# Optimization experiments

Measured on AMD Instinct MI355X. Metric: run time of the kernel, lower is better.

The kernel has to match this reference:

```python
import jax, jax.numpy as jnp
import numpy as np

B, S, R, C_Q, C_KV, H, C_A = 1, 128, 256, 256, 256, 8, 32


def setup_inputs() -> dict:
    key = jax.random.key(0)
    ks = jax.random.split(key, 11)
    scale = 0.02
    q = jax.random.normal(ks[0], (B, S, R, C_Q), jnp.float32)
    kv = jax.random.normal(ks[1], (B, S, R, C_KV), jnp.float32)
    bias = jax.random.normal(ks[2], (B, 1, R, R, H), jnp.float32)
    bias_mask = jax.random.randint(ks[3], (B, S, R), 0, 2).astype(jnp.float32)
    w_q = jax.random.normal(ks[4], (C_Q, H, C_A), jnp.float32) * scale
    w_k = jax.random.normal(ks[5], (C_KV, H, C_A), jnp.float32) * scale
    w_v = jax.random.normal(ks[6], (C_KV, H, C_A), jnp.float32) * scale
    w_g = jax.random.normal(ks[7], (C_Q, H, C_A), jnp.float32) * scale
    b_g = jax.random.normal(ks[8], (H, C_A), jnp.float32) * scale
    w_o = jax.random.normal(ks[9], (H, C_A, C_Q), jnp.float32) * scale
    b_o = jax.random.normal(ks[10], (C_Q,), jnp.float32) * scale
    return {"q": q, "kv": kv, "bias": bias, "bias_mask": bias_mask,
            "w_q": w_q, "w_k": w_k, "w_v": w_v, "w_g": w_g, "b_g": b_g,
            "w_o": w_o, "b_o": b_o}


def reference(q, kv, bias, bias_mask, w_q, w_k, w_v, w_g, b_g, w_o, b_o):
    # q, kv: [B, S, R, C]; attention over residue dim R within each row s.
    c_a = w_q.shape[-1]
    normsize = 1.0 / jnp.sqrt(jnp.asarray(c_a, q.dtype))
    Q = jnp.einsum('bsqc,chd->bsqhd', q, w_q) * normsize  # [B,S,R,H,Ca]
    K = jnp.einsum('bskc,chd->bskhd', kv, w_k)
    V = jnp.einsum('bskc,chd->bskhd', kv, w_v)
    # affinity: [B,S,Q,K,H]
    AT = jnp.einsum('bsqhd,bskhd->bsqkh', Q, K)
    mask_bias = (bias_mask[:, :, None, :, None] - 1.0) * 1e9  # [B,S,1,K,1]
    AT = AT + bias + mask_bias
    AT = jax.nn.softmax(AT, axis=-2)  # softmax over K
    O = jnp.einsum('bsqkh,bskhd->bsqhd', AT, V)
    G = jax.nn.sigmoid(jnp.einsum('bsqc,chd->bsqhd', q, w_g) + b_g)
    O = O * G
    out = jnp.einsum('bsqhd,hdc->bsqc', O, w_o) + b_o  # [B,S,R,C_Q]
    return out
```

## Files before the change

### kernel.cpp

```cpp
#include <hip/hip_runtime.h>

typedef __bf16 bf16;
typedef __bf16 bf16x8 __attribute__((ext_vector_type(8)));
typedef __bf16 bf16x4 __attribute__((ext_vector_type(4)));
typedef float  f32x4  __attribute__((ext_vector_type(4)));
typedef unsigned int u32;
typedef unsigned int u32x2 __attribute__((ext_vector_type(2)));
typedef unsigned int u32x4 __attribute__((ext_vector_type(4)));
typedef unsigned short u16;

#define MFMA16(a, b, c) __builtin_amdgcn_mfma_f32_16x16x32_bf16((a), (b), (c), 0, 0, 0)
#define L2E 1.4426950408889634f


typedef __attribute__((address_space(3))) u32 lds_u32;
typedef const __attribute__((address_space(1))) u32 glob_u32;
__device__ __forceinline__ void gll16(const void* g, void* l) {
    __builtin_amdgcn_global_load_lds((glob_u32*)g, (lds_u32*)l, 16, 0, 0);
}

__device__ __forceinline__ u32 pk2(float lo, float hi) {
    u16 a = __builtin_bit_cast(u16, (bf16)lo);
    u16 b = __builtin_bit_cast(u16, (bf16)hi);
    return ((u32)b << 16) | (u32)a;
}

__device__ __forceinline__ float fexp2(float x) {
#if __has_builtin(__builtin_amdgcn_exp2f)
    return __builtin_amdgcn_exp2f(x);
#else
    return exp2f(x);
#endif
}

__global__ __launch_bounds__(256) void prep_kernel(
    const float* __restrict__ q, const float* __restrict__ kv,
    const float* __restrict__ bias,
    const float* __restrict__ w_q, const float* __restrict__ w_k,
    const float* __restrict__ w_v, const float* __restrict__ w_g,
    const float* __restrict__ w_o,
    bf16* __restrict__ qbf, bf16* __restrict__ kvbf, float* __restrict__ biasT,
    bf16* __restrict__ Wqg, bf16* __restrict__ Wkv, bf16* __restrict__ Wo)
{
    const float norm = 0.17677669529663687f * L2E;
    const int gid = blockIdx.x * 256 + threadIdx.x;
    const int gsz = gridDim.x * 256;

    for (int u = gid; u < 2097152; u += gsz) {
        const float* src; bf16* dst;
        if (u < 1048576) { src = q + (size_t)u * 8;            dst = qbf  + (size_t)u * 8; }
        else             { src = kv + (size_t)(u - 1048576)*8; dst = kvbf + (size_t)(u - 1048576)*8; }
        float4 x0 = *(const float4*)(src);
        float4 x1 = *(const float4*)(src + 4);
        bf16x8 t;
        t[0]=(bf16)x0.x; t[1]=(bf16)x0.y; t[2]=(bf16)x0.z; t[3]=(bf16)x0.w;
        t[4]=(bf16)x1.x; t[5]=(bf16)x1.y; t[6]=(bf16)x1.z; t[7]=(bf16)x1.w;
        *(bf16x8*)dst = t;
    }
    for (int u = gid; u < 524288; u += gsz) {
        int h = u >> 16, qq = (u >> 8) & 255, kk = u & 255;
        biasT[u] = bias[(((qq << 8) + kk) << 3) + h] * L2E;
    }
    for (int u = gid; u < 131072; u += gsz) {
        int n = u >> 8, k = u & 255;
        float v = (n < 256) ? w_q[k * 256 + n] * norm : w_g[k * 256 + (n - 256)];
        Wqg[u] = (bf16)v;
    }
    for (int u = gid; u < 131072; u += gsz) {
        int n = u >> 8, k = u & 255;
        float v = (n < 256) ? w_k[k * 256 + n] : w_v[k * 256 + (n - 256)];
        Wkv[u] = (bf16)v;
    }
    for (int u = gid; u < 65536; u += gsz) {
        int n = u >> 8, k = u & 255;
        Wo[u] = (bf16)w_o[k * 256 + n];
    }
}

template<bool F32OUT>
__device__ __forceinline__ void gemm_core(
    const bf16* __restrict__ A, const bf16* __restrict__ Bw,
    bf16* __restrict__ Cb, float* __restrict__ Cf, const float* __restrict__ bo,
    int m0, int n0, int ntot)
{
    __shared__ __align__(16) bf16 As[128 * 32];
    __shared__ __align__(16) bf16 Bs[128 * 32];

    const int tid  = threadIdx.x;
    const int lane = tid & 63, wave = tid >> 6;
    const int quad = lane >> 4, lc = lane & 15;
    const int wr = wave >> 1, wc = wave & 1;

    const int r0 = tid >> 2, p0 = tid & 3;
    const bf16* gA0 = A  + (size_t)(m0 + r0) * 256 + p0 * 8;
    const bf16* gA1 = A  + (size_t)(m0 + 64 + r0) * 256 + p0 * 8;
    const bf16* gB0 = Bw + (size_t)(n0 + r0) * 256 + p0 * 8;
    const bf16* gB1 = Bw + (size_t)(n0 + 64 + r0) * 256 + p0 * 8;
    bf16* lA0 = As + tid * 8;
    bf16* lA1 = As + (tid + 256) * 8;
    bf16* lB0 = Bs + tid * 8;
    bf16* lB1 = Bs + (tid + 256) * 8;

    f32x4 acc[4][4];
    #pragma unroll
    for (int i = 0; i < 4; ++i)
        #pragma unroll
        for (int j = 0; j < 4; ++j) acc[i][j] = f32x4{0.f, 0.f, 0.f, 0.f};

    #pragma unroll 1
    for (int kb = 0; kb < 8; ++kb) {
        const int ko = kb * 32;
        gll16(gA0 + ko, lA0);
        gll16(gA1 + ko, lA1);
        gll16(gB0 + ko, lB0);
        gll16(gB1 + ko, lB1);
        __syncthreads();

        bf16x8 aF[4], bF[4];
        #pragma unroll
        for (int mt = 0; mt < 4; ++mt)
            aF[mt] = *(const bf16x8*)(As + (wr * 64 + mt * 16 + lc) * 32 + quad * 8);
        #pragma unroll
        for (int nt = 0; nt < 4; ++nt)
            bF[nt] = *(const bf16x8*)(Bs + (wc * 64 + nt * 16 + lc) * 32 + quad * 8);
        #pragma unroll
        for (int mt = 0; mt < 4; ++mt)
            #pragma unroll
            for (int nt = 0; nt < 4; ++nt)
                acc[mt][nt] = MFMA16(aF[mt], bF[nt], acc[mt][nt]);
        __syncthreads();
    }

    #pragma unroll
    for (int mt = 0; mt < 4; ++mt) {
        #pragma unroll
        for (int nt = 0; nt < 4; ++nt) {
            const int row = m0 + wr * 64 + mt * 16 + quad * 4;
            const int col = n0 + wc * 64 + nt * 16 + lc;
            if (F32OUT) {
                float b = bo[col];
                #pragma unroll
                for (int rr = 0; rr < 4; ++rr)
                    Cf[(size_t)(row + rr) * ntot + col] = acc[mt][nt][rr] + b;
            } else {
                #pragma unroll
                for (int rr = 0; rr < 4; ++rr)
                    Cb[(size_t)(row + rr) * ntot + col] = (bf16)acc[mt][nt][rr];
            }
        }
    }
}

__global__ __launch_bounds__(256) void proj_kernel(
    const bf16* __restrict__ qbf, const bf16* __restrict__ kvbf,
    const bf16* __restrict__ Wqg, const bf16* __restrict__ Wkv,
    bf16* __restrict__ QG, bf16* __restrict__ KV)
{
    int bid = blockIdx.x;
    bool sel = bid >= 1024;
    int b = sel ? bid - 1024 : bid;
    int m0 = (b & 255) * 128, n0 = (b >> 8) * 128;
    gemm_core<false>(sel ? kvbf : qbf, sel ? Wkv : Wqg,
                     sel ? KV : QG, nullptr, nullptr, m0, n0, 512);
}

__global__ __launch_bounds__(256) void outproj_kernel(
    const bf16* __restrict__ OG, const bf16* __restrict__ Wo,
    const float* __restrict__ bo, float* __restrict__ out)
{
    int b = blockIdx.x;
    int m0 = (b & 255) * 128, n0 = (b >> 8) * 128;
    gemm_core<true>(OG, Wo, nullptr, out, bo, m0, n0, 256);
}

#define A_OFF_MASK 0
#define A_OFF_K    1024
#define A_OFF_VT   21504
#define A_LDS_TOT  (21504 + 32 * 264 * 2)

__global__ __launch_bounds__(256) void attn_kernel(
    const bf16* __restrict__ QG, const bf16* __restrict__ KV,
    const float* __restrict__ biasT, const float* __restrict__ bias_mask,
    const float* __restrict__ b_g, bf16* __restrict__ OG)
{
    __shared__ __align__(16) char smem[A_LDS_TOT];
    float* maskadd = (float*)(smem + A_OFF_MASK);
    bf16*  Ks      = (bf16*)(smem + A_OFF_K);
    bf16*  Vt      = (bf16*)(smem + A_OFF_VT);

    const int tid  = threadIdx.x;
    const int wave = tid >> 6, lane = tid & 63;
    const int quad = lane >> 4, lc = lane & 15;
    const int h = blockIdx.x >> 7;
    const int s = blockIdx.x & 127;

    maskadd[tid] = (bias_mask[s * 256 + tid] - 1.0f) * (1e9f * L2E);
    {
        const bf16* kvrow = KV + (size_t)(s * 256 + tid) * 512 + h * 32;
        #pragma unroll
        for (int j = 0; j < 4; ++j)
            *(bf16x8*)(Ks + tid * 40 + j * 8) = *(const bf16x8*)(kvrow + j * 8);
        bf16x8 vx[4];
        #pragma unroll
        for (int j = 0; j < 4; ++j) vx[j] = *(const bf16x8*)(kvrow + 256 + j * 8);
        #pragma unroll
        for (int d = 0; d < 32; ++d)
            Vt[d * 264 + tid] = vx[d >> 3][d & 7];
    }
    __syncthreads();

    #pragma unroll 1
    for (int p = 0; p < 4; ++p) {
        const int q0 = (wave * 4 + p) * 16;

        bf16x8 qf = *(const bf16x8*)(QG + (size_t)(s * 256 + q0 + lc) * 512 + h * 32 + quad * 8);

        const float* bT = biasT + (((size_t)h * 256 + q0 + lc) << 8) + quad * 4;
        u32x2 cw[16];
        float sum = 0.f;
        #pragma unroll
        for (int half = 0; half < 2; ++half) {
            f32x4 sc[8];
            #pragma unroll
            for (int k8 = 0; k8 < 8; ++k8) {
                const int kt = half * 8 + k8;
                bf16x8 kf = *(const bf16x8*)(Ks + (kt * 16 + lc) * 40 + quad * 8);
                f32x4 z = {0.f, 0.f, 0.f, 0.f};
                sc[k8] = MFMA16(kf, qf, z);
            }
            #pragma unroll
            for (int k8 = 0; k8 < 8; ++k8) {
                const int kt = half * 8 + k8;
                f32x4 bv = *(const f32x4*)(bT + kt * 16);
                f32x4 mv = *(const f32x4*)(maskadd + kt * 16 + quad * 4);
                float e0 = fexp2(sc[k8][0] + bv[0] + mv[0]);
                float e1 = fexp2(sc[k8][1] + bv[1] + mv[1]);
                float e2 = fexp2(sc[k8][2] + bv[2] + mv[2]);
                float e3 = fexp2(sc[k8][3] + bv[3] + mv[3]);
                sum += (e0 + e1) + (e2 + e3);
                cw[kt] = u32x2{pk2(e0, e1), pk2(e2, e3)};
            }
            __builtin_amdgcn_sched_barrier(0);
        }

        const bf16* gp = QG + (size_t)(s * 256 + q0 + lc) * 512 + 256 + h * 32 + quad * 4;
        bf16x4 gv0 = *(const bf16x4*)(gp);
        bf16x4 gv1 = *(const bf16x4*)(gp + 16);

        f32x4 o0 = {0.f, 0.f, 0.f, 0.f}, o1 = {0.f, 0.f, 0.f, 0.f};
        #pragma unroll
        for (int ks = 0; ks < 8; ++ks) {
            u32 c0 = cw[2 * ks].x,     c1 = cw[2 * ks].y;
            u32 c2 = cw[2 * ks + 1].x, c3 = cw[2 * ks + 1].y;
            u32x2 s02 = __builtin_amdgcn_permlane32_swap(c0, c2, false, false);
            u32x2 s13 = __builtin_amdgcn_permlane32_swap(c1, c3, false, false);
            u32x2 e02 = __builtin_amdgcn_permlane16_swap(s02.x, s02.y, false, false);
            u32x2 e13 = __builtin_amdgcn_permlane16_swap(s13.x, s13.y, false, false);
            u32x4 pw = {e02.x, e13.x, e02.y, e13.y};
            bf16x8 pf = __builtin_bit_cast(bf16x8, pw);
            bf16x8 v0 = *(const bf16x8*)(Vt + lc * 264 + ks * 32 + quad * 8);
            bf16x8 v1 = *(const bf16x8*)(Vt + (16 + lc) * 264 + ks * 32 + quad * 8);
            o0 = MFMA16(v0, pf, o0);
            o1 = MFMA16(v1, pf, o1);
        }

        sum += __shfl_xor(sum, 16, 64);
        sum += __shfl_xor(sum, 32, 64);
        const float inv = 1.0f / sum;

        const f32x4 bg0 = *(const f32x4*)(b_g + h * 32 + quad * 4);
        const f32x4 bg1 = *(const f32x4*)(b_g + h * 32 + 16 + quad * 4);
        bf16* op = OG + (size_t)(s * 256 + q0 + lc) * 256 + h * 32 + quad * 4;
        #pragma unroll
        for (int nt = 0; nt < 2; ++nt) {
            f32x4 ov = nt ? o1 : o0;
            f32x4 bg = nt ? bg1 : bg0;
            bf16x4 gv = nt ? gv1 : gv0;
            bf16x4 ob;
            #pragma unroll
            for (int rr = 0; rr < 4; ++rr) {
                float g = 1.0f / (1.0f + __expf(-((float)gv[rr] + bg[rr])));
                ob[rr] = (bf16)(ov[rr] * inv * g);
            }
            *(bf16x4*)(op + nt * 16) = ob;
        }
    }
}

extern "C" void kernel_launch(void* const* d_in, const int* in_sizes, int n_in,
                              void* d_out, int out_size, void* d_ws, size_t ws_size,
                              hipStream_t stream)
{
    (void)in_sizes; (void)n_in; (void)out_size; (void)ws_size;
    const float* q    = (const float*)d_in[0];
    const float* kv   = (const float*)d_in[1];
    const float* bias = (const float*)d_in[2];
    const float* mask = (const float*)d_in[3];
    const float* w_q  = (const float*)d_in[4];
    const float* w_k  = (const float*)d_in[5];
    const float* w_v  = (const float*)d_in[6];
    const float* w_g  = (const float*)d_in[7];
    const float* b_g  = (const float*)d_in[8];
    const float* w_o  = (const float*)d_in[9];
    const float* b_o  = (const float*)d_in[10];
    float* out = (float*)d_out;

    char* ws = (char*)d_ws;
    bf16*  qbf   = (bf16*)(ws + 0);
    bf16*  kvbf  = (bf16*)(ws + 16777216);
    bf16*  QG    = (bf16*)(ws + 33554432);
    bf16*  KV    = (bf16*)(ws + 67108864);
    float* biasT = (float*)(ws + 100663296);
    bf16*  Wqg   = (bf16*)(ws + 102760448);
    bf16*  Wkv   = (bf16*)(ws + 103022592);
    bf16*  Wo    = (bf16*)(ws + 103284736);
    bf16*  OG    = qbf;

    prep_kernel<<<1024, 256, 0, stream>>>(q, kv, bias, w_q, w_k, w_v, w_g, w_o,
                                          qbf, kvbf, biasT, Wqg, Wkv, Wo);
    proj_kernel<<<2048, 256, 0, stream>>>(qbf, kvbf, Wqg, Wkv, QG, KV);
    attn_kernel<<<1024, 256, 0, stream>>>(QG, KV, biasT, mask, b_g, OG);
    outproj_kernel<<<512, 256, 0, stream>>>(OG, Wo, b_o, out);
}
```

Baseline: 214.1 us.

## Fuse fp32-to-bf16 input conversion into projection GEMM and tidy attention epilogue

Drops the separate pass that converted q and kv to bf16 in the prep kernel. The projection GEMM now reads fp32 activations directly and converts them while staging into LDS, which removes a full write and re-read of 32MB of bf16 intermediates. The gate weights and bias are pre-scaled by log2(e) so the sigmoid can use exp2 and a hardware reciprocal, and the gate bias load is hoisted out of the loop. The trade-off is that the A operand no longer uses async global-to-LDS loads, so the GEMM reads twice the bytes per tile through registers, with less overlap. The prep grid is also made smaller.

```diff
diff --git a/kernel.cpp b/kernel.cpp
--- a/kernel.cpp
+++ b/kernel.cpp
@@ -32,38 +32,34 @@
     return exp2f(x);
 #endif
 }
+__device__ __forceinline__ float frcp(float x) {
+#if __has_builtin(__builtin_amdgcn_rcpf)
+    return __builtin_amdgcn_rcpf(x);
+#else
+    return 1.0f / x;
+#endif
+}
 
 __global__ __launch_bounds__(256) void prep_kernel(
-    const float* __restrict__ q, const float* __restrict__ kv,
     const float* __restrict__ bias,
     const float* __restrict__ w_q, const float* __restrict__ w_k,
     const float* __restrict__ w_v, const float* __restrict__ w_g,
-    const float* __restrict__ w_o,
-    bf16* __restrict__ qbf, bf16* __restrict__ kvbf, float* __restrict__ biasT,
-    bf16* __restrict__ Wqg, bf16* __restrict__ Wkv, bf16* __restrict__ Wo)
+    const float* __restrict__ w_o, const float* __restrict__ b_g,
+    float* __restrict__ biasT,
+    bf16* __restrict__ Wqg, bf16* __restrict__ Wkv, bf16* __restrict__ Wo,
+    float* __restrict__ b_gL)
 {
     const float norm = 0.17677669529663687f * L2E;
     const int gid = blockIdx.x * 256 + threadIdx.x;
     const int gsz = gridDim.x * 256;
 
-    for (int u = gid; u < 2097152; u += gsz) {
-        const float* src; bf16* dst;
-        if (u < 1048576) { src = q + (size_t)u * 8;            dst = qbf  + (size_t)u * 8; }
-        else             { src = kv + (size_t)(u - 1048576)*8; dst = kvbf + (size_t)(u - 1048576)*8; }
-        float4 x0 = *(const float4*)(src);
-        float4 x1 = *(const float4*)(src + 4);
-        bf16x8 t;
-        t[0]=(bf16)x0.x; t[1]=(bf16)x0.y; t[2]=(bf16)x0.z; t[3]=(bf16)x0.w;
-        t[4]=(bf16)x1.x; t[5]=(bf16)x1.y; t[6]=(bf16)x1.z; t[7]=(bf16)x1.w;
-        *(bf16x8*)dst = t;
-    }
     for (int u = gid; u < 524288; u += gsz) {
         int h = u >> 16, qq = (u >> 8) & 255, kk = u & 255;
         biasT[u] = bias[(((qq << 8) + kk) << 3) + h] * L2E;
     }
     for (int u = gid; u < 131072; u += gsz) {
         int n = u >> 8, k = u & 255;
-        float v = (n < 256) ? w_q[k * 256 + n] * norm : w_g[k * 256 + (n - 256)];
+        float v = (n < 256) ? w_q[k * 256 + n] * norm : w_g[k * 256 + (n - 256)] * L2E;
         Wqg[u] = (bf16)v;
     }
     for (int u = gid; u < 131072; u += gsz) {
@@ -75,16 +71,20 @@
         int n = u >> 8, k = u & 255;
         Wo[u] = (bf16)w_o[k * 256 + n];
     }
-}
-
-template<bool F32OUT>
+    for (int u = gid; u < 256; u += gsz) b_gL[u] = b_g[u] * L2E;
+}
+
+template<int AMODE, bool F32OUT>
 __device__ __forceinline__ void gemm_core(
-    const bf16* __restrict__ A, const bf16* __restrict__ Bw,
+    const void* __restrict__ Ap, const bf16* __restrict__ Bw,
     bf16* __restrict__ Cb, float* __restrict__ Cf, const float* __restrict__ bo,
     int m0, int n0, int ntot)
 {
     __shared__ __align__(16) bf16 As[128 * 32];
     __shared__ __align__(16) bf16 Bs[128 * 32];
+
+    const bf16*  A16 = (const bf16*)Ap;
+    const float* A32 = (const float*)Ap;
 
     const int tid  = threadIdx.x;
     const int lane = tid & 63, wave = tid >> 6;
@@ -92,8 +92,8 @@
     const int wr = wave >> 1, wc = wave & 1;
 
     const int r0 = tid >> 2, p0 = tid & 3;
-    const bf16* gA0 = A  + (size_t)(m0 + r0) * 256 + p0 * 8;
-    const bf16* gA1 = A  + (size_t)(m0 + 64 + r0) * 256 + p0 * 8;
+    const size_t offA0 = (size_t)(m0 + r0) * 256 + p0 * 8;
+    const size_t offA1 = (size_t)(m0 + 64 + r0) * 256 + p0 * 8;
     const bf16* gB0 = Bw + (size_t)(n0 + r0) * 256 + p0 * 8;
     const bf16* gB1 = Bw + (size_t)(n0 + 64 + r0) * 256 + p0 * 8;
     bf16* lA0 = As + tid * 8;
@@ -110,10 +110,26 @@
     #pragma unroll 1
     for (int kb = 0; kb < 8; ++kb) {
         const int ko = kb * 32;
-        gll16(gA0 + ko, lA0);
-        gll16(gA1 + ko, lA1);
-        gll16(gB0 + ko, lB0);
-        gll16(gB1 + ko, lB1);
+        if constexpr (AMODE == 0) {
+            gll16(A16 + offA0 + ko, lA0);
+            gll16(A16 + offA1 + ko, lA1);
+            gll16(gB0 + ko, lB0);
+            gll16(gB1 + ko, lB1);
+        } else {
+            float4 x0 = *(const float4*)(A32 + offA0 + ko);
+            float4 x1 = *(const float4*)(A32 + offA0 + ko + 4);
+            float4 y0 = *(const float4*)(A32 + offA1 + ko);
+            float4 y1 = *(const float4*)(A32 + offA1 + ko + 4);
+            gll16(gB0 + ko, lB0);
+            gll16(gB1 + ko, lB1);
+            bf16x8 ta, tb;
+            ta[0]=(bf16)x0.x; ta[1]=(bf16)x0.y; ta[2]=(bf16)x0.z; ta[3]=(bf16)x0.w;
+            ta[4]=(bf16)x1.x; ta[5]=(bf16)x1.y; ta[6]=(bf16)x1.z; ta[7]=(bf16)x1.w;
+            tb[0]=(bf16)y0.x; tb[1]=(bf16)y0.y; tb[2]=(bf16)y0.z; tb[3]=(bf16)y0.w;
+            tb[4]=(bf16)y1.x; tb[5]=(bf16)y1.y; tb[6]=(bf16)y1.z; tb[7]=(bf16)y1.w;
+            *(bf16x8*)lA0 = ta;
+            *(bf16x8*)lA1 = tb;
+        }
         __syncthreads();
 
         bf16x8 aF[4], bF[4];
@@ -152,7 +168,7 @@
 }
 
 __global__ __launch_bounds__(256) void proj_kernel(
-    const bf16* __restrict__ qbf, const bf16* __restrict__ kvbf,
+    const float* __restrict__ qf, const float* __restrict__ kvf,
     const bf16* __restrict__ Wqg, const bf16* __restrict__ Wkv,
     bf16* __restrict__ QG, bf16* __restrict__ KV)
 {
@@ -160,8 +176,8 @@
     bool sel = bid >= 1024;
     int b = sel ? bid - 1024 : bid;
     int m0 = (b & 255) * 128, n0 = (b >> 8) * 128;
-    gemm_core<false>(sel ? kvbf : qbf, sel ? Wkv : Wqg,
-                     sel ? KV : QG, nullptr, nullptr, m0, n0, 512);
+    gemm_core<1, false>(sel ? kvf : qf, sel ? Wkv : Wqg,
+                        sel ? KV : QG, nullptr, nullptr, m0, n0, 512);
 }
 
 __global__ __launch_bounds__(256) void outproj_kernel(
@@ -170,7 +186,7 @@
 {
     int b = blockIdx.x;
     int m0 = (b & 255) * 128, n0 = (b >> 8) * 128;
-    gemm_core<true>(OG, Wo, nullptr, out, bo, m0, n0, 256);
+    gemm_core<0, true>(OG, Wo, nullptr, out, bo, m0, n0, 256);
 }
 
 #define A_OFF_MASK 0
@@ -181,7 +197,7 @@
 __global__ __launch_bounds__(256) void attn_kernel(
     const bf16* __restrict__ QG, const bf16* __restrict__ KV,
     const float* __restrict__ biasT, const float* __restrict__ bias_mask,
-    const float* __restrict__ b_g, bf16* __restrict__ OG)
+    const float* __restrict__ b_gL, bf16* __restrict__ OG)
 {
     __shared__ __align__(16) char smem[A_LDS_TOT];
     float* maskadd = (float*)(smem + A_OFF_MASK);
@@ -208,6 +224,9 @@
             Vt[d * 264 + tid] = vx[d >> 3][d & 7];
     }
     __syncthreads();
+
+    const f32x4 bg0 = *(const f32x4*)(b_gL + h * 32 + quad * 4);
+    const f32x4 bg1 = *(const f32x4*)(b_gL + h * 32 + 16 + quad * 4);
 
     #pragma unroll 1
     for (int p = 0; p < 4; ++p) {
@@ -233,14 +252,15 @@
                 const int kt = half * 8 + k8;
                 f32x4 bv = *(const f32x4*)(bT + kt * 16);
                 f32x4 mv = *(const f32x4*)(maskadd + kt * 16 + quad * 4);
-                float e0 = fexp2(sc[k8][0] + bv[0] + mv[0]);
-                float e1 = fexp2(sc[k8][1] + bv[1] + mv[1]);
-                float e2 = fexp2(sc[k8][2] + bv[2] + mv[2]);
-                float e3 = fexp2(sc[k8][3] + bv[3] + mv[3]);
+                f32x4 t = sc[k8] + bv + mv;
+                float e0 = fexp2(t[0]);
+                float e1 = fexp2(t[1]);
+                float e2 = fexp2(t[2]);
+                float e3 = fexp2(t[3]);
                 sum += (e0 + e1) + (e2 + e3);
                 cw[kt] = u32x2{pk2(e0, e1), pk2(e2, e3)};
             }
-            __builtin_amdgcn_sched_barrier(0);
+            __builtin_amdgcn_sched_barrier(0x6);
         }
 
         const bf16* gp = QG + (size_t)(s * 256 + q0 + lc) * 512 + 256 + h * 32 + quad * 4;
@@ -266,10 +286,8 @@
 
         sum += __shfl_xor(sum, 16, 64);
         sum += __shfl_xor(sum, 32, 64);
-        const float inv = 1.0f / sum;
-
-        const f32x4 bg0 = *(const f32x4*)(b_g + h * 32 + quad * 4);
-        const f32x4 bg1 = *(const f32x4*)(b_g + h * 32 + 16 + quad * 4);
+        const float inv = frcp(sum);
+
         bf16* op = OG + (size_t)(s * 256 + q0 + lc) * 256 + h * 32 + quad * 4;
         #pragma unroll
         for (int nt = 0; nt < 2; ++nt) {
@@ -279,8 +297,9 @@
             bf16x4 ob;
             #pragma unroll
             for (int rr = 0; rr < 4; ++rr) {
-                float g = 1.0f / (1.0f + __expf(-((float)gv[rr] + bg[rr])));
-                ob[rr] = (bf16)(ov[rr] * inv * g);
+                float e = fexp2(-((float)gv[rr] + bg[rr]));
+                float g = frcp(1.0f + e);
+                ob[rr] = (bf16)(ov[rr] * (inv * g));
             }
             *(bf16x4*)(op + nt * 16) = ob;
         }
@@ -306,19 +325,18 @@
     float* out = (float*)d_out;
 
     char* ws = (char*)d_ws;
-    bf16*  qbf   = (bf16*)(ws + 0);
-    bf16*  kvbf  = (bf16*)(ws + 16777216);
+    bf16*  OG    = (bf16*)(ws + 0);
     bf16*  QG    = (bf16*)(ws + 33554432);
     bf16*  KV    = (bf16*)(ws + 67108864);
     float* biasT = (float*)(ws + 100663296);
     bf16*  Wqg   = (bf16*)(ws + 102760448);
     bf16*  Wkv   = (bf16*)(ws + 103022592);
     bf16*  Wo    = (bf16*)(ws + 103284736);
-    bf16*  OG    = qbf;
-
-    prep_kernel<<<1024, 256, 0, stream>>>(q, kv, bias, w_q, w_k, w_v, w_g, w_o,
-                                          qbf, kvbf, biasT, Wqg, Wkv, Wo);
-    proj_kernel<<<2048, 256, 0, stream>>>(qbf, kvbf, Wqg, Wkv, QG, KV);
-    attn_kernel<<<1024, 256, 0, stream>>>(QG, KV, biasT, mask, b_g, OG);
+    float* b_gL  = (float*)(ws + 103415808);
+
+    prep_kernel<<<256, 256, 0, stream>>>(bias, w_q, w_k, w_v, w_g, w_o, b_g,
+                                         biasT, Wqg, Wkv, Wo, b_gL);
+    proj_kernel<<<2048, 256, 0, stream>>>(q, kv, Wqg, Wkv, QG, KV);
+    attn_kernel<<<1024, 256, 0, stream>>>(QG, KV, biasT, mask, b_gL, OG);
     outproj_kernel<<<512, 256, 0, stream>>>(OG, Wo, b_o, out);
 }
```

Result: no change. 213.0 us (-0.5%).
